# Optimization experiments

Hardware: AMD Instinct MI355X
Metric: run time of the kernel (lower is better)

The kernel has to match this reference:

```python
import jax, jax.numpy as jnp
import numpy as np

MD = 20          # max_displacement
TEMP = 1e-4      # softmax temperature
B, C, H, W = 4, 64, 112, 112


def setup_inputs() -> dict:
    key = jax.random.key(0)
    k1, k2 = jax.random.split(key)
    in1 = jax.random.normal(k1, (B, C, H, W), dtype=jnp.float32)
    in2 = jax.random.normal(k2, (B, C, H, W), dtype=jnp.float32)
    return {"in1": in1, "in2": in2}


def reference(in1, in2):
    b, c, h, w = in1.shape
    # F.normalize(x, dim=1): x / max(||x||_2, eps)
    def l2n(x):
        return x / jnp.maximum(jnp.linalg.norm(x, axis=1, keepdims=True), 1e-12)
    in1 = l2n(in1)
    in2 = l2n(in2)

    pad = jnp.pad(in2, ((0, 0), (0, 0), (MD, MD), (MD, MD)))

    d = jnp.arange(-MD, MD + 1)
    dx, dy = jnp.meshgrid(d, d, indexing="ij")  # torch.meshgrid default 'ij'
    dx = dx.reshape(-1)  # [K] with K = (2*MD+1)^2
    dy = dy.reshape(-1)

    def sim_one(dxi, dyi):
        # shifted window of padded in2, same spatial size as in1
        sl = jax.lax.dynamic_slice(pad, (0, 0, MD + dxi, MD + dyi), (b, c, h, w))
        return jnp.sum(in1 * sl, axis=1)  # [B,H,W]

    sim = jax.vmap(sim_one)(dx, dy)          # [K,B,H,W]
    sim = jnp.transpose(sim, (1, 0, 2, 3))   # [B,K,H,W] cost volume

    weights = jax.nn.softmax(sim / TEMP, axis=1)  # softmax over displacements
    guide = jnp.stack((dx, dy), axis=-1).astype(jnp.float32)  # [K,2]
    # flow[b,d,h,w] = sum_k weights[b,k,h,w] * guide[k,d]
    flow = jnp.einsum("bkhw,kd->bdhw", weights, guide)
    return flow
```

## Files before the change

### kernel.cpp

```cpp
#include <hip/hip_runtime.h>

#define BB 4
#define CC 64
#define HH 112
#define WW 112
#define MD 20
#define KD 41
#define S2 14426.950408f
#define NT 10
#define ROW2 (NT*2*2*64*8)

typedef _Float16 half8   __attribute__((ext_vector_type(8)));
typedef float    f32x4   __attribute__((ext_vector_type(4)));
typedef unsigned short ushort8 __attribute__((ext_vector_type(8)));

static __device__ __forceinline__ float fmax_f(float a, float b) { return a > b ? a : b; }
static __device__ __forceinline__ unsigned short f2h_bits(float x) {
    _Float16 h = (_Float16)x;
    return __builtin_bit_cast(unsigned short, h);
}
static __device__ __forceinline__ float h2f(unsigned short s) {
    return (float)__builtin_bit_cast(_Float16, s);
}
static __device__ __forceinline__ f32x4 vmax4(f32x4 a, f32x4 b) {
    f32x4 r;
    #pragma unroll
    for (int k = 0; k < 4; ++k) r[k] = a[k] > b[k] ? a[k] : b[k];
    return r;
}
static __device__ __forceinline__ f32x4 vexp4(f32x4 d) {
    f32x4 r;
    #pragma unroll
    for (int k = 0; k < 4; ++k) r[k] = __builtin_amdgcn_exp2f(d[k]);
    return r;
}
static __device__ __forceinline__ f32x4 mfma16(half8 a, half8 b, f32x4 c) {
    return __builtin_amdgcn_mfma_f32_16x16x32_f16(a, b, c, 0, 0, 0);
}

__global__ __launch_bounds__(256) void pack_kernel(const float* __restrict__ in2,
                                                   unsigned short* __restrict__ in2s) {
    __shared__ float tile[CC][WW + 1];
    __shared__ float sinv[WW];
    int b = blockIdx.x / HH, h = blockIdx.x % HH;
    int t = threadIdx.x;
    const float* src = in2 + ((size_t)(b*CC)*HH + h)*WW;

    for (int i = t; i < CC*WW; i += 256) {
        int c = i / WW, w = i % WW;
        tile[c][w] = src[(size_t)c*(HH*WW) + w];
    }
    __syncthreads();
    if (t < WW) {
        float s = 0.f;
        #pragma unroll
        for (int c = 0; c < CC; ++c) { float x = tile[c][t]; s += x*x; }
        sinv[t] = 1.0f / fmax_f(__builtin_sqrtf(s), 1e-12f);
    }
    __syncthreads();

    int wv = t >> 6, lane = t & 63;
    int n = lane & 15, q = lane >> 4;
    unsigned short* base = in2s + (size_t)(b*HH + h)*ROW2;
    for (int u = wv; u < NT*2; u += 4) {
        int tau = u >> 1, ks = u & 1;
        int col = 16*tau + n - MD;
        ushort8 hb = {0,0,0,0,0,0,0,0}, lb = {0,0,0,0,0,0,0,0};
        if (col >= 0 && col < WW) {
            float iv = sinv[col];
            #pragma unroll
            for (int j = 0; j < 8; ++j) {
                int c = 32*ks + 8*q + j;
                float x = tile[c][col] * iv;
                unsigned short xh = f2h_bits(x);
                hb[j] = xh;
                lb[j] = f2h_bits((x - h2f(xh)) * 4096.0f);
            }
        }
        *(ushort8*)(base + (size_t)((tau*4 + ks*2 + 0)*64 + lane)*8) = hb;
        *(ushort8*)(base + (size_t)((tau*4 + ks*2 + 1)*64 + lane)*8) = lb;
    }
}

__global__ __launch_bounds__(128) void corr_kernel(const float* __restrict__ in1,
                                                   const unsigned short* __restrict__ in2s,
                                                   float* __restrict__ out) {
    int gid = blockIdx.x;
    int xcd = gid & 7;
    int s   = gid >> 3;
    int b   = xcd >> 1;
    int p   = (xcd & 1)*28 + (s % 28);
    int wt  = s / 28;
    int wv  = threadIdx.x >> 6;
    int h   = p + 56*wv;
    int lane = threadIdx.x & 63;
    int n = lane & 15, q = lane >> 4;
    int m0 = 4*q;
    int wA = wt*16 + n;

    const float* a_src = in1 + ((size_t)(b*CC)*HH + h)*WW + wA;
    float x[16];
    float ss = 0.f;
    #pragma unroll
    for (int ks = 0; ks < 2; ++ks)
        #pragma unroll
        for (int j = 0; j < 8; ++j) {
            float v = a_src[(size_t)(32*ks + 8*q + j)*(HH*WW)];
            x[ks*8 + j] = v;
            ss += v*v;
        }
    ss += __shfl_xor(ss, 16);
    ss += __shfl_xor(ss, 32);
    float i1 = 1.0f / fmax_f(__builtin_sqrtf(ss), 1e-12f);
    half8 aH[2], aL[2];
    #pragma unroll
    for (int ks = 0; ks < 2; ++ks)
        #pragma unroll
        for (int j = 0; j < 8; ++j) {
            float v = x[ks*8 + j] * i1;
            _Float16 vh = (_Float16)v;
            aH[ks][j] = vh;
            aL[ks][j] = (_Float16)((v - (float)vh) * 4096.0f);
        }

    f32x4 NM20; bool v0b[4], v2b[4], v3b[4];
    #pragma unroll
    for (int r = 0; r < 4; ++r) {
        int nm = n - (m0 + r);
        NM20[r] = (float)(nm - 20);
        v0b[r] = (nm >= 0);
        v2b[r] = (nm <= 8);
        v3b[r] = (nm <= -8);
    }

    f32x4 SM = {-4.f,-4.f,-4.f,-4.f}, SL = {0.f,0.f,0.f,0.f};
    f32x4 SSX = {0.f,0.f,0.f,0.f}, SSY = {0.f,0.f,0.f,0.f};

    int dlo = MD - h > 0 ? MD - h : 0;
    int dhi = (HH + MD - h) < KD ? (HH + MD - h) : KD;

    for (int dxi = dlo; dxi < dhi; ++dxi) {
        const unsigned short* rb = in2s + (size_t)(b*HH + (h + dxi - MD))*ROW2;
        half8 bf[4][4];
        #pragma unroll
        for (int oi = 0; oi < 4; ++oi) {
            const half8* fp = (const half8*)(rb + (size_t)((wt + oi)*4*64 + lane)*8);
            bf[oi][0] = fp[0];
            bf[oi][1] = fp[64];
            bf[oi][2] = fp[128];
            bf[oi][3] = fp[192];
        }
        f32x4 sv[4];
        #pragma unroll
        for (int oi = 0; oi < 4; ++oi) {
            f32x4 a0 = {0.f,0.f,0.f,0.f}, a1 = {0.f,0.f,0.f,0.f};
            a0 = mfma16(aH[0], bf[oi][0], a0);
            a1 = mfma16(aH[0], bf[oi][1], a1);
            a1 = mfma16(aL[0], bf[oi][0], a1);
            a0 = mfma16(aH[1], bf[oi][2], a0);
            a1 = mfma16(aH[1], bf[oi][3], a1);
            a1 = mfma16(aL[1], bf[oi][2], a1);
            sv[oi] = a0 + a1 * (1.0f/4096.0f);
        }
        f32x4 V0, V1 = sv[1], V2, V3;
        #pragma unroll
        for (int r = 0; r < 4; ++r) {
            V0[r] = v0b[r] ? sv[0][r] : -4.0f;
            V2[r] = v2b[r] ? sv[2][r] : -4.0f;
            V3[r] = v3b[r] ? sv[3][r] : -4.0f;
        }
        f32x4 MN = vmax4(vmax4(SM, V0), vmax4(V1, vmax4(V2, V3)));
        f32x4 ER = vexp4((SM - MN) * S2);
        f32x4 E0 = vexp4((V0 - MN) * S2);
        f32x4 E1 = vexp4((V1 - MN) * S2);
        f32x4 E2 = vexp4((V2 - MN) * S2);
        f32x4 E3 = vexp4((V3 - MN) * S2);
        f32x4 SUM = (E0 + E1) + (E2 + E3);
        f32x4 TT  = E1 + E2*2.0f + E3*3.0f;
        float dxf = (float)(dxi - MD);
        SL  = SL *ER + SUM;
        SSX = SSX*ER + SUM*dxf;
        SSY = SSY*ER + (TT*16.0f + NM20*SUM);
        SM  = MN;
    }

    int miss = dlo + (KD - dhi);
    if (miss > 0) {
        float sdx = 0.f;
        for (int d = 0; d < dlo; ++d)  sdx += (float)(d - MD);
        for (int d = dhi; d < KD; ++d) sdx += (float)(d - MD);
        float cnt = (float)miss * (float)KD;
        f32x4 Z = {0.f,0.f,0.f,0.f};
        f32x4 MN = vmax4(SM, Z);
        f32x4 ER = vexp4((SM - MN) * S2);
        f32x4 E0 = vexp4((Z  - MN) * S2);
        SL  = SL *ER + E0*cnt;
        SSX = SSX*ER + E0*((float)KD*sdx);
        SSY = SSY*ER;
        SM  = MN;
    }

    #pragma unroll
    for (int off = 1; off < 16; off <<= 1) {
        f32x4 M2, L2, X2, Y2;
        #pragma unroll
        for (int k = 0; k < 4; ++k) {
            M2[k] = __shfl_xor(SM[k],  off);
            L2[k] = __shfl_xor(SL[k],  off);
            X2[k] = __shfl_xor(SSX[k], off);
            Y2[k] = __shfl_xor(SSY[k], off);
        }
        f32x4 MN = vmax4(SM, M2);
        f32x4 EA = vexp4((SM - MN) * S2);
        f32x4 EB = vexp4((M2 - MN) * S2);
        SL  = SL *EA + L2*EB;
        SSX = SSX*EA + X2*EB;
        SSY = SSY*EA + Y2*EB;
        SM  = MN;
    }

    if (n == 0) {
        #pragma unroll
        for (int r = 0; r < 4; ++r) {
            int w = wt*16 + m0 + r;
            out[((b*2 + 0)*HH + h)*WW + w] = SSX[r] / SL[r];
            out[((b*2 + 1)*HH + h)*WW + w] = SSY[r] / SL[r];
        }
    }
}

extern "C" void kernel_launch(void* const* d_in, const int* in_sizes, int n_in,
                              void* d_out, int out_size, void* d_ws, size_t ws_size,
                              hipStream_t stream) {
    const float* in1 = (const float*)d_in[0];
    const float* in2 = (const float*)d_in[1];
    float* out = (float*)d_out;
    unsigned short* in2s = (unsigned short*)d_ws;

    pack_kernel<<<BB*HH, 256, 0, stream>>>(in2, in2s);
    corr_kernel<<<8*196, 128, 0, stream>>>(in1, in2s, out);
}
```

Measured before the change: 165.2 us.

## Split displacement rows across blocks, merge partial softmax, repack without LDS

The correlation kernel now splits the 41 vertical displacements into three groups of 14. Each block covers one row with 7 width-tile waves and writes partial online-softmax state (max, sum, x/y moments) to workspace. A new merge kernel combines the three partials into the flow. The pack kernel drops its LDS tile and computes the norm per wave with shuffles, and the temperature scale is folded into the MFMA output so it is no longer applied inside every exp. This adds parallelism and removes the serial dependence along dx, but costs an extra kernel launch, partial-state traffic, and a larger workspace.

```diff
diff --git a/kernel.cpp b/kernel.cpp
--- a/kernel.cpp
+++ b/kernel.cpp
@@ -7,8 +7,11 @@
 #define MD 20
 #define KD 41
 #define S2 14426.950408f
+#define NPIX (BB*HH*WW)
 #define NT 10
 #define ROW2 (NT*2*2*64*8)
+#define IN2S_BYTES ((size_t)BB*HH*ROW2*2)
+#define NEG (-60000.0f)
 
 typedef _Float16 half8   __attribute__((ext_vector_type(8)));
 typedef float    f32x4   __attribute__((ext_vector_type(4)));
@@ -40,59 +43,58 @@
 
 __global__ __launch_bounds__(256) void pack_kernel(const float* __restrict__ in2,
                                                    unsigned short* __restrict__ in2s) {
-    __shared__ float tile[CC][WW + 1];
-    __shared__ float sinv[WW];
-    int b = blockIdx.x / HH, h = blockIdx.x % HH;
-    int t = threadIdx.x;
-    const float* src = in2 + ((size_t)(b*CC)*HH + h)*WW;
-
-    for (int i = t; i < CC*WW; i += 256) {
-        int c = i / WW, w = i % WW;
-        tile[c][w] = src[(size_t)c*(HH*WW) + w];
-    }
-    __syncthreads();
-    if (t < WW) {
-        float s = 0.f;
-        #pragma unroll
-        for (int c = 0; c < CC; ++c) { float x = tile[c][t]; s += x*x; }
-        sinv[t] = 1.0f / fmax_f(__builtin_sqrtf(s), 1e-12f);
-    }
-    __syncthreads();
-
-    int wv = t >> 6, lane = t & 63;
+    int wid = blockIdx.x*4 + (threadIdx.x >> 6);
+    int lane = threadIdx.x & 63;
+    int tau = wid % NT;
+    int bh  = wid / NT;
+    int b = bh / HH, h = bh % HH;
     int n = lane & 15, q = lane >> 4;
+    int col = 16*tau + n - MD;
+    bool ok = (col >= 0 && col < WW);
+    int colc = ok ? col : 0;
+    const float* src = in2 + ((size_t)(b*CC)*HH + h)*WW + colc;
+
+    float x[16];
+    float ss = 0.f;
+    #pragma unroll
+    for (int ks = 0; ks < 2; ++ks)
+        #pragma unroll
+        for (int j = 0; j < 8; ++j) {
+            float v = ok ? src[(size_t)(32*ks + 8*q + j)*(HH*WW)] : 0.f;
+            x[ks*8 + j] = v;
+            ss += v*v;
+        }
+    ss += __shfl_xor(ss, 16);
+    ss += __shfl_xor(ss, 32);
+    float iv = 1.0f / fmax_f(__builtin_sqrtf(ss), 1e-12f);
+
     unsigned short* base = in2s + (size_t)(b*HH + h)*ROW2;
-    for (int u = wv; u < NT*2; u += 4) {
-        int tau = u >> 1, ks = u & 1;
-        int col = 16*tau + n - MD;
-        ushort8 hb = {0,0,0,0,0,0,0,0}, lb = {0,0,0,0,0,0,0,0};
-        if (col >= 0 && col < WW) {
-            float iv = sinv[col];
-            #pragma unroll
-            for (int j = 0; j < 8; ++j) {
-                int c = 32*ks + 8*q + j;
-                float x = tile[c][col] * iv;
-                unsigned short xh = f2h_bits(x);
-                hb[j] = xh;
-                lb[j] = f2h_bits((x - h2f(xh)) * 4096.0f);
-            }
+    #pragma unroll
+    for (int ks = 0; ks < 2; ++ks) {
+        ushort8 hb, lb;
+        #pragma unroll
+        for (int j = 0; j < 8; ++j) {
+            float v = x[ks*8 + j] * iv;
+            unsigned short vh = f2h_bits(v);
+            hb[j] = vh;
+            lb[j] = f2h_bits((v - h2f(vh)) * 4096.0f);
         }
         *(ushort8*)(base + (size_t)((tau*4 + ks*2 + 0)*64 + lane)*8) = hb;
         *(ushort8*)(base + (size_t)((tau*4 + ks*2 + 1)*64 + lane)*8) = lb;
     }
 }
 
-__global__ __launch_bounds__(128) void corr_kernel(const float* __restrict__ in1,
+__global__ __launch_bounds__(448) void corr_kernel(const float* __restrict__ in1,
                                                    const unsigned short* __restrict__ in2s,
-                                                   float* __restrict__ out) {
+                                                   float* __restrict__ part) {
     int gid = blockIdx.x;
-    int xcd = gid & 7;
-    int s   = gid >> 3;
-    int b   = xcd >> 1;
-    int p   = (xcd & 1)*28 + (s % 28);
-    int wt  = s / 28;
-    int wv  = threadIdx.x >> 6;
-    int h   = p + 56*wv;
+    int xcd  = gid & 7;
+    int slot = gid >> 3;
+    int hloc = slot % 56;
+    int g    = slot / 56;
+    int b    = xcd >> 1;
+    int h    = (xcd & 1)*56 + hloc;
+    int wt   = threadIdx.x >> 6;
     int lane = threadIdx.x & 63;
     int n = lane & 15, q = lane >> 4;
     int m0 = 4*q;
@@ -133,13 +135,17 @@
         v3b[r] = (nm <= -8);
     }
 
-    f32x4 SM = {-4.f,-4.f,-4.f,-4.f}, SL = {0.f,0.f,0.f,0.f};
+    f32x4 SM = {NEG,NEG,NEG,NEG}, SL = {0.f,0.f,0.f,0.f};
     f32x4 SSX = {0.f,0.f,0.f,0.f}, SSY = {0.f,0.f,0.f,0.f};
 
-    int dlo = MD - h > 0 ? MD - h : 0;
-    int dhi = (HH + MD - h) < KD ? (HH + MD - h) : KD;
-
-    for (int dxi = dlo; dxi < dhi; ++dxi) {
+    int glo = g*14;
+    int ghi = glo + 14 < KD ? glo + 14 : KD;
+    int lo = glo > (MD - h) ? glo : (MD - h);
+    int hi0 = HH + MD - h;
+    int hi = ghi < hi0 ? ghi : hi0;
+    if (hi < lo) { lo = ghi; hi = ghi; }
+
+    for (int dxi = lo; dxi < hi; ++dxi) {
         const unsigned short* rb = in2s + (size_t)(b*HH + (h + dxi - MD))*ROW2;
         half8 bf[4][4];
         #pragma unroll
@@ -160,21 +166,21 @@
             a0 = mfma16(aH[1], bf[oi][2], a0);
             a1 = mfma16(aH[1], bf[oi][3], a1);
             a1 = mfma16(aL[1], bf[oi][2], a1);
-            sv[oi] = a0 + a1 * (1.0f/4096.0f);
+            sv[oi] = a0*S2 + a1*(S2/4096.0f);
         }
         f32x4 V0, V1 = sv[1], V2, V3;
         #pragma unroll
         for (int r = 0; r < 4; ++r) {
-            V0[r] = v0b[r] ? sv[0][r] : -4.0f;
-            V2[r] = v2b[r] ? sv[2][r] : -4.0f;
-            V3[r] = v3b[r] ? sv[3][r] : -4.0f;
+            V0[r] = v0b[r] ? sv[0][r] : NEG;
+            V2[r] = v2b[r] ? sv[2][r] : NEG;
+            V3[r] = v3b[r] ? sv[3][r] : NEG;
         }
         f32x4 MN = vmax4(vmax4(SM, V0), vmax4(V1, vmax4(V2, V3)));
-        f32x4 ER = vexp4((SM - MN) * S2);
-        f32x4 E0 = vexp4((V0 - MN) * S2);
-        f32x4 E1 = vexp4((V1 - MN) * S2);
-        f32x4 E2 = vexp4((V2 - MN) * S2);
-        f32x4 E3 = vexp4((V3 - MN) * S2);
+        f32x4 ER = vexp4(SM - MN);
+        f32x4 E0 = vexp4(V0 - MN);
+        f32x4 E1 = vexp4(V1 - MN);
+        f32x4 E2 = vexp4(V2 - MN);
+        f32x4 E3 = vexp4(V3 - MN);
         f32x4 SUM = (E0 + E1) + (E2 + E3);
         f32x4 TT  = E1 + E2*2.0f + E3*3.0f;
         float dxf = (float)(dxi - MD);
@@ -184,16 +190,16 @@
         SM  = MN;
     }
 
-    int miss = dlo + (KD - dhi);
+    int miss = (lo - glo) + (ghi - hi);
     if (miss > 0) {
         float sdx = 0.f;
-        for (int d = 0; d < dlo; ++d)  sdx += (float)(d - MD);
-        for (int d = dhi; d < KD; ++d) sdx += (float)(d - MD);
+        for (int d = glo; d < lo; ++d)  sdx += (float)(d - MD);
+        for (int d = hi; d < ghi; ++d)  sdx += (float)(d - MD);
         float cnt = (float)miss * (float)KD;
         f32x4 Z = {0.f,0.f,0.f,0.f};
         f32x4 MN = vmax4(SM, Z);
-        f32x4 ER = vexp4((SM - MN) * S2);
-        f32x4 E0 = vexp4((Z  - MN) * S2);
+        f32x4 ER = vexp4(SM - MN);
+        f32x4 E0 = vexp4(Z  - MN);
         SL  = SL *ER + E0*cnt;
         SSX = SSX*ER + E0*((float)KD*sdx);
         SSY = SSY*ER;
@@ -211,8 +217,8 @@
             Y2[k] = __shfl_xor(SSY[k], off);
         }
         f32x4 MN = vmax4(SM, M2);
-        f32x4 EA = vexp4((SM - MN) * S2);
-        f32x4 EB = vexp4((M2 - MN) * S2);
+        f32x4 EA = vexp4(SM - MN);
+        f32x4 EB = vexp4(M2 - MN);
         SL  = SL *EA + L2*EB;
         SSX = SSX*EA + X2*EB;
         SSY = SSY*EA + Y2*EB;
@@ -223,10 +229,30 @@
         #pragma unroll
         for (int r = 0; r < 4; ++r) {
             int w = wt*16 + m0 + r;
-            out[((b*2 + 0)*HH + h)*WW + w] = SSX[r] / SL[r];
-            out[((b*2 + 1)*HH + h)*WW + w] = SSY[r] / SL[r];
-        }
-    }
+            int pix = (b*HH + h)*WW + w;
+            float* p = &part[(size_t)(g*NPIX + pix)*4];
+            p[0] = SM[r]; p[1] = SL[r]; p[2] = SSX[r]; p[3] = SSY[r];
+        }
+    }
+}
+
+__global__ __launch_bounds__(256) void merge_kernel(const float* __restrict__ part,
+                                                    float* __restrict__ out) {
+    int idx = blockIdx.x*256 + threadIdx.x;
+    if (idx >= NPIX) return;
+    const float* p0 = &part[(size_t)idx*4];
+    const float* p1 = &part[(size_t)(NPIX + idx)*4];
+    const float* p2 = &part[(size_t)(2*NPIX + idx)*4];
+    float M = fmax_f(fmax_f(p0[0], p1[0]), p2[0]);
+    float e0 = __builtin_amdgcn_exp2f(p0[0] - M);
+    float e1 = __builtin_amdgcn_exp2f(p1[0] - M);
+    float e2 = __builtin_amdgcn_exp2f(p2[0] - M);
+    float L  = p0[1]*e0 + p1[1]*e1 + p2[1]*e2;
+    float SX = p0[2]*e0 + p1[2]*e1 + p2[2]*e2;
+    float SY = p0[3]*e0 + p1[3]*e1 + p2[3]*e2;
+    int b = idx / (HH*WW), rem = idx % (HH*WW);
+    out[(b*2 + 0)*(HH*WW) + rem] = SX / L;
+    out[(b*2 + 1)*(HH*WW) + rem] = SY / L;
 }
 
 extern "C" void kernel_launch(void* const* d_in, const int* in_sizes, int n_in,
@@ -236,7 +262,9 @@
     const float* in2 = (const float*)d_in[1];
     float* out = (float*)d_out;
     unsigned short* in2s = (unsigned short*)d_ws;
-
-    pack_kernel<<<BB*HH, 256, 0, stream>>>(in2, in2s);
-    corr_kernel<<<8*196, 128, 0, stream>>>(in1, in2s, out);
-}
+    float* part = (float*)((char*)d_ws + IN2S_BYTES);
+
+    pack_kernel <<<1120, 256, 0, stream>>>(in2, in2s);
+    corr_kernel <<<1344, 448, 0, stream>>>(in1, in2s, part);
+    merge_kernel<<<(NPIX+255)/256, 256, 0, stream>>>(part, out);
+}
```

Result: faster. 157.3 us (-4.8%).
